# Optimization experiments

Measured on AMD Instinct MI355X. Metric: run time of the kernel, lower is better.

## Reference

```python
import jax, jax.numpy as jnp
import numpy as np

LN_EPS = 1e-5


def _layernorm(x, g, b):
    mu = x.mean(-1, keepdims=True)
    var = x.var(-1, keepdims=True)
    return (x - mu) / jnp.sqrt(var + LN_EPS) * g + b


def _rel_pos_index(p):
    # static numpy computation, identical to the torch buffer
    coords = np.stack(np.meshgrid(np.arange(p), np.arange(p), indexing='ij'))  # (2,p,p)
    flat = coords.reshape(2, -1)  # (2, p*p)
    rel = flat[:, :, None] - flat[:, None, :]  # (2, N, N)
    rel = rel.transpose(1, 2, 0).copy()
    rel[:, :, 0] += p - 1
    rel[:, :, 1] += p - 1
    rel[:, :, 0] *= 2 * p - 1
    return rel.sum(-1)  # (N, N)


def setup_inputs() -> dict:
    key = jax.random.key(0)
    ks = jax.random.split(key, 8)
    B, H, W, C, heads, p = 32, 56, 56, 384, 12, 7
    hid = 4 * C
    s = 0.02
    return {
        'x': jax.random.normal(ks[0], (B, H * W, C), jnp.float32),
        'norm1_g': jnp.ones((C,), jnp.float32),
        'norm1_b': jnp.zeros((C,), jnp.float32),
        'qkv_w': jax.random.normal(ks[1], (3 * C, C), jnp.float32) * s,
        'qkv_b': jnp.zeros((3 * C,), jnp.float32),
        'rpb_table': jax.random.normal(ks[2], ((2 * p - 1) ** 2, heads), jnp.float32) * s,
        'proj_w': jax.random.normal(ks[3], (C, C), jnp.float32) * s,
        'proj_b': jnp.zeros((C,), jnp.float32),
        'norm2_g': jnp.ones((C,), jnp.float32),
        'norm2_b': jnp.zeros((C,), jnp.float32),
        'fc1_w': jax.random.normal(ks[4], (hid, C), jnp.float32) * s,
        'fc1_b': jnp.zeros((hid,), jnp.float32),
        'fc2_w': jax.random.normal(ks[5], (C, hid), jnp.float32) * s,
        'fc2_b': jnp.zeros((C,), jnp.float32),
        'H': H, 'W': W, 'patch_size': p, 'num_heads': heads,
    }


def reference(x, norm1_g, norm1_b, qkv_w, qkv_b, rpb_table, proj_w, proj_b,
              norm2_g, norm2_b, fc1_w, fc1_b, fc2_w, fc2_b,
              H, W, patch_size, num_heads):
    B, L, C = x.shape
    p = patch_size
    N = p * p
    head_dim = C // num_heads
    scale = head_dim ** -0.5

    shortcut = x
    h = _layernorm(x, norm1_g, norm1_b).reshape(B, H, W, C)
    # partition into (B*nWin, N, C); H, W divisible by p so no padding
    h = h.reshape(B, H // p, p, W // p, p, C).transpose(0, 1, 3, 2, 4, 5)
    patches = h.reshape(-1, N, C)
    Bw = patches.shape[0]

    # IPSA attention
    qkv = patches @ qkv_w.T + qkv_b  # (Bw, N, 3C)
    qkv = qkv.reshape(Bw, N, 3, num_heads, head_dim).transpose(2, 0, 3, 1, 4)
    q, k, v = qkv[0] * scale, qkv[1], qkv[2]  # (Bw, h, N, d)
    attn = jnp.einsum('bhnd,bhmd->bhnm', q, k)
    bias = rpb_table[_rel_pos_index(p).reshape(-1)].reshape(N, N, num_heads)
    attn = attn + bias.transpose(2, 0, 1)[None]
    attn = jax.nn.softmax(attn, axis=-1)
    out = jnp.einsum('bhnm,bhmd->bhnd', attn, v).transpose(0, 2, 1, 3).reshape(Bw, N, C)
    out = out @ proj_w.T + proj_b

    # reverse partition
    out = out.reshape(B, H // p, W // p, p, p, C).transpose(0, 1, 3, 2, 4, 5)
    out = out.reshape(B, H * W, C)

    x = shortcut + out
    y = _layernorm(x, norm2_g, norm2_b)
    y = jax.nn.gelu(y @ fc1_w.T + fc1_b, approximate=False)
    y = y @ fc2_w.T + fc2_b
    return x + y
```

## Files before the change

kernel.cpp:

```cpp
#include <hip/hip_runtime.h>
#include <cstdint>
#include <cstddef>

typedef __bf16 bf16;
typedef __bf16 bf16x4 __attribute__((ext_vector_type(4)));
typedef __bf16 bf16x8 __attribute__((ext_vector_type(8)));
typedef float f32x4 __attribute__((ext_vector_type(4)));

static_assert(sizeof(bf16x8) == 16, "bf16x8 must be 16B");

#define NTOK 100352
#define CDIM 384

#define AS1(p) ((const __attribute__((address_space(1))) void*)(p))
#define AS3(p) ((__attribute__((address_space(3))) void*)(p))

__global__ __launch_bounds__(256) void cvt_k(const float* __restrict__ in,
                                             bf16* __restrict__ out, int n)
{
    const int i = (blockIdx.x * 256 + threadIdx.x) * 4;
    if (i < n) {
        const float4 v = *(const float4*)(in + i);
        bf16x4 o;
        o[0] = (bf16)v.x; o[1] = (bf16)v.y; o[2] = (bf16)v.z; o[3] = (bf16)v.w;
        *(bf16x4*)(out + i) = o;
    }
}

__global__ __launch_bounds__(256) void bias_k(const float* __restrict__ rpb,
                                              float* __restrict__ biasE)
{
    const int t = blockIdx.x * 256 + threadIdx.x;
    const int i = t & 63, j = (t >> 6) & 63, hd = t >> 12;
    float v = -3e38f;
    if (i < 49 && j < 49) {
        const int iy = i / 7, ix = i % 7, jy = j / 7, jx = j % 7;
        v = rpb[((jy - iy + 6) * 13 + (jx - ix + 6)) * 12 + hd];
    }
    biasE[t] = v;
}

__global__ __launch_bounds__(256) void ln32_k(const float* __restrict__ x,
    const float* __restrict__ g, const float* __restrict__ b, bf16* __restrict__ y)
{
    const int wave = threadIdx.x >> 6, lane = threadIdx.x & 63;
    const size_t row = (size_t)blockIdx.x * 4 + wave;
    const float2* xr = (const float2*)(x + row * CDIM);
    float v[6];
    float s = 0.f, s2 = 0.f;
#pragma unroll
    for (int i = 0; i < 3; i++) {
        const float2 t = xr[lane + i * 64];
        v[2 * i] = t.x; v[2 * i + 1] = t.y;
        s += t.x + t.y; s2 += t.x * t.x + t.y * t.y;
    }
#pragma unroll
    for (int off = 32; off > 0; off >>= 1) {
        s  += __shfl_xor(s, off);
        s2 += __shfl_xor(s2, off);
    }
    const float mu   = s * (1.f / CDIM);
    const float rstd = rsqrtf(s2 * (1.f / CDIM) - mu * mu + 1e-5f);
    const float2* gu = (const float2*)g;
    const float2* bu = (const float2*)b;
    uint32_t* yu = (uint32_t*)(y + row * CDIM);
#pragma unroll
    for (int i = 0; i < 3; i++) {
        const float2 gg = gu[lane + i * 64], bb = bu[lane + i * 64];
        const float o0 = (v[2 * i] - mu) * rstd * gg.x + bb.x;
        const float o1 = (v[2 * i + 1] - mu) * rstd * gg.y + bb.y;
        const uint32_t pk = (uint32_t)__builtin_bit_cast(unsigned short, (bf16)o0)
                          | ((uint32_t)__builtin_bit_cast(unsigned short, (bf16)o1) << 16);
        yu[lane + i * 64] = pk;
    }
}

template <int EPI, typename TO>
__global__ __launch_bounds__(256) void gemm_bt(
    const bf16* __restrict__ A, const bf16* __restrict__ Bm,
    const float* __restrict__ bias, const float* __restrict__ res,
    TO* __restrict__ Cc, int N, int K)
{
    __shared__ __align__(16) bf16 lds[3][2][128 * 32];
    const int tid = threadIdx.x;

    const int gx = gridDim.x;
    const int nwg = gx * gridDim.y;
    const int orig = blockIdx.y * gx + blockIdx.x;
    const int q = nwg >> 3, r = nwg & 7;
    const int xcd = orig & 7, lid = orig >> 3;
    const int swz = (xcd < r ? xcd * (q + 1) : r * (q + 1) + (xcd - r) * q) + lid;
    const int m0 = (swz / gx) * 128, n0 = (swz % gx) * 128;

    const int wave = tid >> 6, lane = tid & 63;
    const int wm = (wave >> 1) * 64, wn = (wave & 1) * 64;
    const int lm = lane & 15;
    const int lko = (((lane >> 4) ^ ((lm >> 1) & 3)) & 3) * 8;

    const int sr = tid >> 2;
    const int sc = (((tid & 3) ^ ((sr >> 1) & 3)) & 3) * 8;

    const bf16* Ap0 = A + (size_t)(m0 + sr) * K + sc;
    const bf16* Ap1 = A + (size_t)(m0 + sr + 64) * K + sc;
    const bf16* Bp0 = Bm + (size_t)(n0 + sr) * K + sc;
    const bf16* Bp1 = Bm + (size_t)(n0 + sr + 64) * K + sc;

#define STAGE(buf, koff) do {                                                           \
    __builtin_amdgcn_global_load_lds(AS1(Ap0 + (koff)),                                 \
        AS3(&lds[buf][0][(wave * 16) * 32]), 16, 0, 0);                                 \
    __builtin_amdgcn_global_load_lds(AS1(Ap1 + (koff)),                                 \
        AS3(&lds[buf][0][(64 + wave * 16) * 32]), 16, 0, 0);                            \
    __builtin_amdgcn_global_load_lds(AS1(Bp0 + (koff)),                                 \
        AS3(&lds[buf][1][(wave * 16) * 32]), 16, 0, 0);                                 \
    __builtin_amdgcn_global_load_lds(AS1(Bp1 + (koff)),                                 \
        AS3(&lds[buf][1][(64 + wave * 16) * 32]), 16, 0, 0);                            \
} while (0)

    f32x4 acc[4][4] = {};

    const int nt = K >> 5;
    STAGE(0, 0);
    STAGE(1, 32);
    int bi = 0;
    for (int t = 0; t < nt; ++t) {
        if (t + 2 < nt) {
            const int b2 = bi ? bi - 1 : 2;
            STAGE(b2, (t + 2) << 5);
            asm volatile("s_waitcnt vmcnt(8)" ::: "memory");
        } else if (t + 1 < nt) {
            asm volatile("s_waitcnt vmcnt(4)" ::: "memory");
        } else {
            asm volatile("s_waitcnt vmcnt(0)" ::: "memory");
        }
        __builtin_amdgcn_sched_barrier(0);
        __builtin_amdgcn_s_barrier();
        bf16x8 af[4], bfr[4];
#pragma unroll
        for (int i = 0; i < 4; i++)
            af[i] = *(const bf16x8*)&lds[bi][0][(wm + i * 16 + lm) * 32 + lko];
#pragma unroll
        for (int i = 0; i < 4; i++)
            bfr[i] = *(const bf16x8*)&lds[bi][1][(wn + i * 16 + lm) * 32 + lko];
#pragma unroll
        for (int mi = 0; mi < 4; mi++)
#pragma unroll
            for (int ni = 0; ni < 4; ni++)
                acc[mi][ni] = __builtin_amdgcn_mfma_f32_16x16x32_bf16(
                    af[mi], bfr[ni], acc[mi][ni], 0, 0, 0);
        if (t + 1 < nt) {
            __builtin_amdgcn_sched_barrier(0);
            __builtin_amdgcn_s_barrier();
        }
        bi = (bi == 2) ? 0 : bi + 1;
    }
#undef STAGE

    if (EPI == 2) {
        const int rb = m0 + wm + (lane >> 4) * 4;
        const int cb = n0 + wn + lm;
#pragma unroll
        for (int ni = 0; ni < 4; ni++) {
            const int col = cb + ni * 16;
            const float bv = bias[col];
#pragma unroll
            for (int mi = 0; mi < 4; mi++) {
#pragma unroll
                for (int r2 = 0; r2 < 4; r2++) {
                    const int row = rb + mi * 16 + r2;
                    float v = acc[mi][ni][r2] + bv;
                    v += res[(size_t)row * N + col];
                    Cc[(size_t)row * N + col] = (TO)v;
                }
            }
        }
    } else {
        __syncthreads();
        bf16* Ct = (bf16*)lds;
        const int rbl = wm + (lane >> 4) * 4;
        const int cbl = wn + lm;
#pragma unroll
        for (int ni = 0; ni < 4; ni++) {
            const float bv = bias[n0 + cbl + ni * 16];
#pragma unroll
            for (int mi = 0; mi < 4; mi++) {
#pragma unroll
                for (int r2 = 0; r2 < 4; r2++) {
                    float v = acc[mi][ni][r2] + bv;
                    if (EPI == 1) {
                        const float p  = fmaf(v * v, 0.07135481627f, 1.59576912161f);
                        const float u2 = fminf(v * p, 80.f);
                        const float e  = __expf(u2);
                        v = v * e * __builtin_amdgcn_rcpf(1.f + e);
                    }
                    Ct[(rbl + mi * 16 + r2) * 128 + cbl + ni * 16] = (bf16)v;
                }
            }
        }
        __syncthreads();
#pragma unroll
        for (int c2 = 0; c2 < 8; ++c2) {
            const int chunk = tid + (c2 << 8);
            const int row = chunk >> 4, c8 = (chunk & 15) << 3;
            *(bf16x8*)((bf16*)Cc + (size_t)(m0 + row) * N + n0 + c8) =
                *(const bf16x8*)&Ct[row * 128 + c8];
        }
    }
}

__global__ __launch_bounds__(256) void attn_k(const bf16* __restrict__ qkv,
    const float* __restrict__ biasE, bf16* __restrict__ out)
{
    const int w  = blockIdx.x;
    const int bb = w >> 6, win = w & 63, wy = win >> 3, wx = win & 7;
    __shared__ int toks[64];
    __shared__ __align__(16) bf16 VT[4][32 * 64];
    __shared__ __align__(16) bf16 P[4][64 * 64];
    const int tid = threadIdx.x;
    if (tid < 64) {
        const int t = tid < 49 ? tid : 48;
        toks[tid] = bb * 3136 + (wy * 7 + t / 7) * 56 + wx * 7 + t % 7;
    }
    __syncthreads();

    const int wave = tid >> 6, lane = tid & 63;
    const int g = lane >> 4, lr = lane & 15;
    char* vt = (char*)VT[wave];
    char* pb = (char*)P[wave];

    for (int hh = 0; hh < 3; ++hh) {
        const int hd = wave * 3 + hh;
#pragma unroll
        for (int c = 0; c < 4; ++c) {
            const int idx = c * 64 + lane;
            const int row = idx >> 2, d0 = (idx & 3) * 8;
            if (row < 49) {
                const bf16x8 vv = *(const bf16x8*)(qkv + (size_t)toks[row] * 1152 + 768 + hd * 32 + d0);
#pragma unroll
                for (int e = 0; e < 8; ++e) {
                    const int d = d0 + e;
                    *(bf16*)(vt + (((d * 64 + row) * 2) ^ ((d & 7) << 4))) = vv[e];
                }
            } else {
#pragma unroll
                for (int e = 0; e < 8; ++e) {
                    const int d = d0 + e;
                    *(bf16*)(vt + (((d * 64 + row) * 2) ^ ((d & 7) << 4))) = (bf16)0.f;
                }
            }
        }
        bf16x8 kf[4], qf[4];
#pragma unroll
        for (int b = 0; b < 4; ++b) {
            const size_t rk = (size_t)toks[b * 16 + lr] * 1152;
            kf[b] = *(const bf16x8*)(qkv + rk + 384 + hd * 32 + g * 8);
            qf[b] = *(const bf16x8*)(qkv + rk +       hd * 32 + g * 8);
        }
        f32x4 s[4][4] = {};
#pragma unroll
        for (int mi = 0; mi < 4; ++mi)
#pragma unroll
            for (int nj = 0; nj < 4; ++nj)
                s[mi][nj] = __builtin_amdgcn_mfma_f32_16x16x32_bf16(kf[mi], qf[nj], s[mi][nj], 0, 0, 0);
        const float* bh = biasE + hd * 4096;
#pragma unroll
        for (int nj = 0; nj < 4; ++nj) {
            const int j = nj * 16 + lr;
            const float* bj = bh + j * 64 + g * 4;
            float mx = -3e38f;
#pragma unroll
            for (int mi = 0; mi < 4; ++mi) {
                const float4 be = *(const float4*)(bj + mi * 16);
                const float* bp4 = (const float*)&be;
#pragma unroll
                for (int r2 = 0; r2 < 4; ++r2) {
                    const float v = fmaf(s[mi][nj][r2], 0.1767766952966369f, bp4[r2]);
                    s[mi][nj][r2] = v;
                    mx = fmaxf(mx, v);
                }
            }
            mx = fmaxf(mx, __shfl_xor(mx, 16));
            mx = fmaxf(mx, __shfl_xor(mx, 32));
            float sm = 0.f;
#pragma unroll
            for (int mi = 0; mi < 4; ++mi)
#pragma unroll
                for (int r2 = 0; r2 < 4; ++r2) {
                    const float e = __expf(s[mi][nj][r2] - mx);
                    s[mi][nj][r2] = e;
                    sm += e;
                }
            sm += __shfl_xor(sm, 16);
            sm += __shfl_xor(sm, 32);
            const float inv = __builtin_amdgcn_rcpf(sm);
#pragma unroll
            for (int mi = 0; mi < 4; ++mi) {
                bf16x4 pk;
#pragma unroll
                for (int r2 = 0; r2 < 4; ++r2) pk[r2] = (bf16)(s[mi][nj][r2] * inv);
                const int i0 = mi * 16 + g * 4;
                *(bf16x4*)(pb + (((j * 64 + i0) * 2) ^ ((j & 7) << 4))) = pk;
            }
        }
        f32x4 o[2][4] = {};
#pragma unroll
        for (int kb = 0; kb < 2; ++kb) {
            bf16x8 av[2], bp[4];
#pragma unroll
            for (int db = 0; db < 2; ++db) {
                const int d = db * 16 + lr;
                av[db] = *(const bf16x8*)(vt + (((d * 64 + kb * 32 + g * 8) * 2) ^ ((d & 7) << 4)));
            }
#pragma unroll
            for (int jb = 0; jb < 4; ++jb) {
                const int j = jb * 16 + lr;
                bp[jb] = *(const bf16x8*)(pb + (((j * 64 + kb * 32 + g * 8) * 2) ^ ((j & 7) << 4)));
            }
#pragma unroll
            for (int db = 0; db < 2; ++db)
#pragma unroll
                for (int jb = 0; jb < 4; ++jb)
                    o[db][jb] = __builtin_amdgcn_mfma_f32_16x16x32_bf16(av[db], bp[jb], o[db][jb], 0, 0, 0);
        }
#pragma unroll
        for (int jb = 0; jb < 4; ++jb) {
            const int j = jb * 16 + lr;
            if (j < 49) {
                bf16* op = out + (size_t)toks[j] * CDIM + hd * 32 + g * 4;
#pragma unroll
                for (int db = 0; db < 2; ++db) {
                    bf16x4 pk;
#pragma unroll
                    for (int r2 = 0; r2 < 4; ++r2) pk[r2] = (bf16)o[db][jb][r2];
                    *(bf16x4*)(op + db * 16) = pk;
                }
            }
        }
    }
}

extern "C" void kernel_launch(void* const* d_in, const int* in_sizes, int n_in,
                              void* d_out, int out_size, void* d_ws, size_t ws_size,
                              hipStream_t stream) {
    const float* x      = (const float*)d_in[0];
    const float* n1g    = (const float*)d_in[1];
    const float* n1b    = (const float*)d_in[2];
    const float* qkv_w  = (const float*)d_in[3];
    const float* qkv_b  = (const float*)d_in[4];
    const float* rpb    = (const float*)d_in[5];
    const float* proj_w = (const float*)d_in[6];
    const float* proj_b = (const float*)d_in[7];
    const float* n2g    = (const float*)d_in[8];
    const float* n2b    = (const float*)d_in[9];
    const float* fc1_w  = (const float*)d_in[10];
    const float* fc1_b  = (const float*)d_in[11];
    const float* fc2_w  = (const float*)d_in[12];
    const float* fc2_b  = (const float*)d_in[13];
    float* out = (float*)d_out;

    const size_t wBytes = 3538944 + 196608;
    int nc = 16;
    for (int c : {1, 2, 4, 8}) {
        if (wBytes + ((size_t)NTOK / c) * 3840 <= ws_size) { nc = c; break; }
    }
    const int rowsC = NTOK / nc;
    const int imgsC = 32 / nc;

    char* ws = (char*)d_ws;
    bf16* wqkv  = (bf16*)ws;
    bf16* wproj = wqkv + 442368;
    bf16* wfc1  = wproj + 147456;
    bf16* wfc2  = wfc1 + 589824;
    float* biasE = (float*)(ws + 3538944);
    bf16* bufH  = (bf16*)(ws + wBytes);
    bf16* bufB  = bufH + (size_t)rowsC * CDIM;
    float* x1   = out;

    cvt_k<<<442368 / 1024, 256, 0, stream>>>(qkv_w, wqkv, 442368);
    cvt_k<<<147456 / 1024, 256, 0, stream>>>(proj_w, wproj, 147456);
    cvt_k<<<589824 / 1024, 256, 0, stream>>>(fc1_w, wfc1, 589824);
    cvt_k<<<589824 / 1024, 256, 0, stream>>>(fc2_w, wfc2, 589824);
    bias_k<<<192, 256, 0, stream>>>(rpb, biasE);

    for (int c = 0; c < nc; c++) {
        const size_t ro = (size_t)c * rowsC;
        ln32_k<<<rowsC / 4, 256, 0, stream>>>(x + ro * CDIM, n1g, n1b, bufH);
        gemm_bt<0, bf16><<<dim3(1152 / 128, rowsC / 128), 256, 0, stream>>>(
            bufH, wqkv, qkv_b, nullptr, bufB, 1152, 384);
        attn_k<<<dim3(64 * imgsC), 256, 0, stream>>>(bufB, biasE, bufH);
        gemm_bt<2, float><<<dim3(384 / 128, rowsC / 128), 256, 0, stream>>>(
            bufH, wproj, proj_b, x + ro * CDIM, x1 + ro * CDIM, 384, 384);
    }
    for (int c = 0; c < nc; c++) {
        const size_t ro = (size_t)c * rowsC;
        ln32_k<<<rowsC / 4, 256, 0, stream>>>(x1 + ro * CDIM, n2g, n2b, bufH);
        gemm_bt<1, bf16><<<dim3(1536 / 128, rowsC / 128), 256, 0, stream>>>(
            bufH, wfc1, fc1_b, nullptr, bufB, 1536, 384);
        gemm_bt<2, float><<<dim3(384 / 128, rowsC / 128), 256, 0, stream>>>(
            bufB, wfc2, fc2_b, x1 + ro * CDIM, out + ro * CDIM, 384, 1536);
    }
}
```

Before: 1.079 ms.

## Enlarge GEMM tile to 256x128 with per-wave 64x128 and single-barrier pipeline

```diff
diff --git a/kernel.cpp b/kernel.cpp
--- a/kernel.cpp
+++ b/kernel.cpp
@@ -76,12 +76,12 @@
 }
 
 template <int EPI, typename TO>
-__global__ __launch_bounds__(256) void gemm_bt(
+__global__ __launch_bounds__(256, 2) void gemm_bt(
     const bf16* __restrict__ A, const bf16* __restrict__ Bm,
     const float* __restrict__ bias, const float* __restrict__ res,
     TO* __restrict__ Cc, int N, int K)
 {
-    __shared__ __align__(16) bf16 lds[3][2][128 * 32];
+    __shared__ __align__(16) bf16 lds[3][384 * 32];
     const int tid = threadIdx.x;
 
     const int gx = gridDim.x;
@@ -90,10 +90,10 @@
     const int q = nwg >> 3, r = nwg & 7;
     const int xcd = orig & 7, lid = orig >> 3;
     const int swz = (xcd < r ? xcd * (q + 1) : r * (q + 1) + (xcd - r) * q) + lid;
-    const int m0 = (swz / gx) * 128, n0 = (swz % gx) * 128;
+    const int m0 = (swz / gx) * 256, n0 = (swz % gx) * 128;
 
     const int wave = tid >> 6, lane = tid & 63;
-    const int wm = (wave >> 1) * 64, wn = (wave & 1) * 64;
+    const int wm = wave * 64;
     const int lm = lane & 15;
     const int lko = (((lane >> 4) ^ ((lm >> 1) & 3)) & 3) * 8;
 
@@ -101,73 +101,72 @@
     const int sc = (((tid & 3) ^ ((sr >> 1) & 3)) & 3) * 8;
 
     const bf16* Ap0 = A + (size_t)(m0 + sr) * K + sc;
-    const bf16* Ap1 = A + (size_t)(m0 + sr + 64) * K + sc;
+    const bf16* Ap1 = A + (size_t)(m0 + 64 + sr) * K + sc;
+    const bf16* Ap2 = A + (size_t)(m0 + 128 + sr) * K + sc;
+    const bf16* Ap3 = A + (size_t)(m0 + 192 + sr) * K + sc;
     const bf16* Bp0 = Bm + (size_t)(n0 + sr) * K + sc;
-    const bf16* Bp1 = Bm + (size_t)(n0 + sr + 64) * K + sc;
-
-#define STAGE(buf, koff) do {                                                           \
-    __builtin_amdgcn_global_load_lds(AS1(Ap0 + (koff)),                                 \
-        AS3(&lds[buf][0][(wave * 16) * 32]), 16, 0, 0);                                 \
-    __builtin_amdgcn_global_load_lds(AS1(Ap1 + (koff)),                                 \
-        AS3(&lds[buf][0][(64 + wave * 16) * 32]), 16, 0, 0);                            \
-    __builtin_amdgcn_global_load_lds(AS1(Bp0 + (koff)),                                 \
-        AS3(&lds[buf][1][(wave * 16) * 32]), 16, 0, 0);                                 \
-    __builtin_amdgcn_global_load_lds(AS1(Bp1 + (koff)),                                 \
-        AS3(&lds[buf][1][(64 + wave * 16) * 32]), 16, 0, 0);                            \
+    const bf16* Bp1 = Bm + (size_t)(n0 + 64 + sr) * K + sc;
+
+#define STAGE(buf, koff) do {                                                            \
+    __builtin_amdgcn_global_load_lds(AS1(Ap0 + (koff)),                                  \
+        AS3(&lds[buf][(  0 + wave * 16) * 32]), 16, 0, 0);                               \
+    __builtin_amdgcn_global_load_lds(AS1(Ap1 + (koff)),                                  \
+        AS3(&lds[buf][( 64 + wave * 16) * 32]), 16, 0, 0);                               \
+    __builtin_amdgcn_global_load_lds(AS1(Ap2 + (koff)),                                  \
+        AS3(&lds[buf][(128 + wave * 16) * 32]), 16, 0, 0);                               \
+    __builtin_amdgcn_global_load_lds(AS1(Ap3 + (koff)),                                  \
+        AS3(&lds[buf][(192 + wave * 16) * 32]), 16, 0, 0);                               \
+    __builtin_amdgcn_global_load_lds(AS1(Bp0 + (koff)),                                  \
+        AS3(&lds[buf][(256 + wave * 16) * 32]), 16, 0, 0);                               \
+    __builtin_amdgcn_global_load_lds(AS1(Bp1 + (koff)),                                  \
+        AS3(&lds[buf][(320 + wave * 16) * 32]), 16, 0, 0);                               \
 } while (0)
 
-    f32x4 acc[4][4] = {};
+    f32x4 acc[4][8] = {};
 
     const int nt = K >> 5;
     STAGE(0, 0);
-    STAGE(1, 32);
     int bi = 0;
     for (int t = 0; t < nt; ++t) {
-        if (t + 2 < nt) {
-            const int b2 = bi ? bi - 1 : 2;
-            STAGE(b2, (t + 2) << 5);
-            asm volatile("s_waitcnt vmcnt(8)" ::: "memory");
-        } else if (t + 1 < nt) {
-            asm volatile("s_waitcnt vmcnt(4)" ::: "memory");
+        if (t + 1 < nt) {
+            const int bn = (bi == 2) ? 0 : bi + 1;
+            STAGE(bn, (t + 1) << 5);
+            asm volatile("s_waitcnt vmcnt(6)" ::: "memory");
         } else {
             asm volatile("s_waitcnt vmcnt(0)" ::: "memory");
         }
+        __builtin_amdgcn_s_barrier();
         __builtin_amdgcn_sched_barrier(0);
-        __builtin_amdgcn_s_barrier();
-        bf16x8 af[4], bfr[4];
+        bf16x8 af[4], bfr[8];
 #pragma unroll
         for (int i = 0; i < 4; i++)
-            af[i] = *(const bf16x8*)&lds[bi][0][(wm + i * 16 + lm) * 32 + lko];
-#pragma unroll
-        for (int i = 0; i < 4; i++)
-            bfr[i] = *(const bf16x8*)&lds[bi][1][(wn + i * 16 + lm) * 32 + lko];
+            af[i] = *(const bf16x8*)&lds[bi][(wm + i * 16 + lm) * 32 + lko];
+#pragma unroll
+        for (int j = 0; j < 8; j++)
+            bfr[j] = *(const bf16x8*)&lds[bi][(256 + j * 16 + lm) * 32 + lko];
 #pragma unroll
         for (int mi = 0; mi < 4; mi++)
 #pragma unroll
-            for (int ni = 0; ni < 4; ni++)
-                acc[mi][ni] = __builtin_amdgcn_mfma_f32_16x16x32_bf16(
-                    af[mi], bfr[ni], acc[mi][ni], 0, 0, 0);
-        if (t + 1 < nt) {
-            __builtin_amdgcn_sched_barrier(0);
-            __builtin_amdgcn_s_barrier();
-        }
+            for (int nj = 0; nj < 8; nj++)
+                acc[mi][nj] = __builtin_amdgcn_mfma_f32_16x16x32_bf16(
+                    af[mi], bfr[nj], acc[mi][nj], 0, 0, 0);
         bi = (bi == 2) ? 0 : bi + 1;
     }
 #undef STAGE
 
     if (EPI == 2) {
         const int rb = m0 + wm + (lane >> 4) * 4;
-        const int cb = n0 + wn + lm;
-#pragma unroll
-        for (int ni = 0; ni < 4; ni++) {
-            const int col = cb + ni * 16;
+        const int cb = n0 + lm;
+#pragma unroll
+        for (int nj = 0; nj < 8; nj++) {
+            const int col = cb + nj * 16;
             const float bv = bias[col];
 #pragma unroll
             for (int mi = 0; mi < 4; mi++) {
 #pragma unroll
                 for (int r2 = 0; r2 < 4; r2++) {
                     const int row = rb + mi * 16 + r2;
-                    float v = acc[mi][ni][r2] + bv;
+                    float v = acc[mi][nj][r2] + bv;
                     v += res[(size_t)row * N + col];
                     Cc[(size_t)row * N + col] = (TO)v;
                 }
@@ -177,28 +176,27 @@
         __syncthreads();
         bf16* Ct = (bf16*)lds;
         const int rbl = wm + (lane >> 4) * 4;
-        const int cbl = wn + lm;
-#pragma unroll
-        for (int ni = 0; ni < 4; ni++) {
-            const float bv = bias[n0 + cbl + ni * 16];
+#pragma unroll
+        for (int nj = 0; nj < 8; nj++) {
+            const float bv = bias[n0 + lm + nj * 16];
 #pragma unroll
             for (int mi = 0; mi < 4; mi++) {
 #pragma unroll
                 for (int r2 = 0; r2 < 4; r2++) {
-                    float v = acc[mi][ni][r2] + bv;
+                    float v = acc[mi][nj][r2] + bv;
                     if (EPI == 1) {
                         const float p  = fmaf(v * v, 0.07135481627f, 1.59576912161f);
                         const float u2 = fminf(v * p, 80.f);
                         const float e  = __expf(u2);
                         v = v * e * __builtin_amdgcn_rcpf(1.f + e);
                     }
-                    Ct[(rbl + mi * 16 + r2) * 128 + cbl + ni * 16] = (bf16)v;
+                    Ct[(rbl + mi * 16 + r2) * 128 + lm + nj * 16] = (bf16)v;
                 }
             }
         }
         __syncthreads();
 #pragma unroll
-        for (int c2 = 0; c2 < 8; ++c2) {
+        for (int c2 = 0; c2 < 16; ++c2) {
             const int chunk = tid + (c2 << 8);
             const int row = chunk >> 4, c8 = (chunk & 15) << 3;
             *(bf16x8*)((bf16*)Cc + (size_t)(m0 + row) * N + n0 + c8) =
@@ -358,7 +356,7 @@
     float* out = (float*)d_out;
 
     const size_t wBytes = 3538944 + 196608;
-    int nc = 16;
+    int nc = 8;
     for (int c : {1, 2, 4, 8}) {
         if (wBytes + ((size_t)NTOK / c) * 3840 <= ws_size) { nc = c; break; }
     }
@@ -384,18 +382,18 @@
     for (int c = 0; c < nc; c++) {
         const size_t ro = (size_t)c * rowsC;
         ln32_k<<<rowsC / 4, 256, 0, stream>>>(x + ro * CDIM, n1g, n1b, bufH);
-        gemm_bt<0, bf16><<<dim3(1152 / 128, rowsC / 128), 256, 0, stream>>>(
+        gemm_bt<0, bf16><<<dim3(1152 / 128, rowsC / 256), 256, 0, stream>>>(
             bufH, wqkv, qkv_b, nullptr, bufB, 1152, 384);
         attn_k<<<dim3(64 * imgsC), 256, 0, stream>>>(bufB, biasE, bufH);
-        gemm_bt<2, float><<<dim3(384 / 128, rowsC / 128), 256, 0, stream>>>(
+        gemm_bt<2, float><<<dim3(384 / 128, rowsC / 256), 256, 0, stream>>>(
             bufH, wproj, proj_b, x + ro * CDIM, x1 + ro * CDIM, 384, 384);
     }
     for (int c = 0; c < nc; c++) {
         const size_t ro = (size_t)c * rowsC;
         ln32_k<<<rowsC / 4, 256, 0, stream>>>(x1 + ro * CDIM, n2g, n2b, bufH);
-        gemm_bt<1, bf16><<<dim3(1536 / 128, rowsC / 128), 256, 0, stream>>>(
+        gemm_bt<1, bf16><<<dim3(1536 / 128, rowsC / 256), 256, 0, stream>>>(
             bufH, wfc1, fc1_b, nullptr, bufB, 1536, 384);
-        gemm_bt<2, float><<<dim3(384 / 128, rowsC / 128), 256, 0, stream>>>(
+        gemm_bt<2, float><<<dim3(384 / 128, rowsC / 256), 256, 0, stream>>>(
             bufB, wfc2, fc2_b, x1 + ro * CDIM, out + ro * CDIM, 384, 1536);
     }
 }
```

New measurement: 1.072 ms. About the same (-0.6%).
